# Performance work log

Hardware: AMD Instinct MI355X
Metric: run time of the kernel (lower is better)

## Reference

```python
import jax, jax.numpy as jnp
import numpy as np

B = 8          # graphs per batch
N_PER = 8192   # nodes per graph (equal-sized graphs -> static topk shapes)
N = B * N_PER  # 65536 total nodes
DEG = 16
E = DEG * N    # 1,048,576 edges
C = 64         # conv_width


def setup_inputs() -> dict:
    key = jax.random.key(0)
    ks = jax.random.split(key, 32)
    epg = E // B
    g = jnp.arange(E, dtype=jnp.int32) // epg            # graph id per edge
    src = jax.random.randint(ks[0], (E,), 0, N_PER, dtype=jnp.int32) + g * N_PER
    dst = jax.random.randint(ks[1], (E,), 0, N_PER, dtype=jnp.int32) + g * N_PER

    def w(k, shape, fan_in):
        return (jax.random.normal(k, shape) / np.sqrt(fan_in)).astype(jnp.float32)

    inp = {
        "x": jax.random.normal(ks[2], (N, 2), dtype=jnp.float32),
        "edge_index": jnp.stack([src, dst]),
        # SAGEConv i: out = mean_agg @ wl + x @ wr + b
        "w1l": w(ks[3], (2, C), 2),  "w1r": w(ks[4], (2, C), 2),  "b1": jnp.zeros((C,), jnp.float32),
        "w2l": w(ks[5], (C, C), C),  "w2r": w(ks[6], (C, C), C),  "b2": jnp.zeros((C,), jnp.float32),
        "w3l": w(ks[7], (C, C), C),  "w3r": w(ks[8], (C, C), C),  "b3": jnp.zeros((C,), jnp.float32),
        # GCNConv
        "w4": w(ks[9], (C, C), C),   "b4": jnp.zeros((C,), jnp.float32),
        # TopKPooling score vectors
        "p1": w(ks[10], (C,), C), "p2": w(ks[11], (C,), C),
        "p3": w(ks[12], (C,), C), "p4": w(ks[13], (C,), C),
        # MLP head
        "lw1": w(ks[14], (2 * C, 128), 2 * C), "lb1": jnp.zeros((128,), jnp.float32),
        "lw2": w(ks[15], (128, 64), 128),      "lb2": jnp.zeros((64,), jnp.float32),
        "lw3": w(ks[16], (64, 1), 64),         "lb3": jnp.zeros((1,), jnp.float32),
    }
    return inp


def _sage(x, src, dst, em, wl, wr, b):
    # PyG SAGEConv: lin_l(mean of in-neighbors) + lin_r(x); masked edges contribute 0
    n = x.shape[0]
    s = jax.ops.segment_sum(x[src] * em[:, None], dst, num_segments=n)
    cnt = jax.ops.segment_sum(em, dst, num_segments=n)
    mean = s / jnp.maximum(cnt, 1.0)[:, None]
    return mean @ wl + x @ wr + b


def _gcn(x, src, dst, em, w, b):
    # PyG GCNConv with added self-loops, symmetric normalization
    n = x.shape[0]
    xw = x @ w
    deg = jax.ops.segment_sum(em, dst, num_segments=n) + 1.0  # +1 self-loop
    dinv = jax.lax.rsqrt(deg)
    coef = (dinv[src] * dinv[dst] * em)[:, None]
    agg = jax.ops.segment_sum(xw[src] * coef, dst, num_segments=n)
    return agg + xw / deg[:, None] + b  # self-loop term: deg^-0.5 * deg^-0.5


def _pool(x, src, dst, em, p, nb):
    # TopKPooling(ratio=0.5): score = x.p/||p||, keep top half per graph, scale by tanh
    n = x.shape[0]
    npg = n // nb
    k = npg // 2
    score = x @ p / jnp.linalg.norm(p)
    _, idx = jax.lax.top_k(score.reshape(nb, npg), k)          # [nb, k] local idx
    perm = (idx + (jnp.arange(nb, dtype=idx.dtype) * npg)[:, None]).reshape(-1)
    xn = x[perm] * jnp.tanh(score[perm])[:, None]
    o2n = jnp.full((n,), -1, jnp.int32).at[perm].set(jnp.arange(nb * k, dtype=jnp.int32))
    ns, nd = o2n[src], o2n[dst]
    nm = em * ((ns >= 0) & (nd >= 0)).astype(em.dtype)         # filter_adj via mask
    return xn, jnp.maximum(ns, 0), jnp.maximum(nd, 0), nm


def _readout(x, nb):
    # cat([global_max_pool, global_mean_pool])
    npg = x.shape[0] // nb
    batch = jnp.repeat(jnp.arange(nb), npg)
    mx = jax.ops.segment_max(x, batch, num_segments=nb)
    mn = jax.ops.segment_sum(x, batch, num_segments=nb) / npg
    return jnp.concatenate([mx, mn], axis=1)


def reference(x, edge_index, w1l, w1r, b1, w2l, w2r, b2, w3l, w3r, b3, w4, b4,
              p1, p2, p3, p4, lw1, lb1, lw2, lb2, lw3, lb3):
    src, dst = edge_index[0], edge_index[1]
    em = jnp.ones((src.shape[0],), jnp.float32)

    h = jax.nn.relu(_sage(x, src, dst, em, w1l, w1r, b1))
    h, src, dst, em = _pool(h, src, dst, em, p1, B)
    x1 = _readout(h, B)

    h = jax.nn.relu(_sage(h, src, dst, em, w2l, w2r, b2))
    h, src, dst, em = _pool(h, src, dst, em, p2, B)
    x2 = _readout(h, B)

    h = jax.nn.relu(_sage(h, src, dst, em, w3l, w3r, b3))
    h, src, dst, em = _pool(h, src, dst, em, p3, B)
    x3 = _readout(h, B)  # computed but unused, matching original (x = x1 + x2)

    h = jax.nn.relu(_gcn(h, src, dst, em, w4, b4))
    h, src, dst, em = _pool(h, src, dst, em, p4, B)
    x4 = _readout(h, B)  # computed but unused, matching original

    z = x1 + x2
    z = jax.nn.relu(z @ lw1 + lb1)
    z = jax.nn.relu(z @ lw2 + lb2)
    return z @ lw3 + lb3  # [B, 1]
```

## Files before the change

### kernel.cpp

```cpp
#include <hip/hip_runtime.h>
#include <stdint.h>
#include <math.h>

#define NB 8
#define NPG0 8192
#define EPG 131072
#define P1 16
#define MAXDEG 64

__global__ __launch_bounds__(1024)
void k_aggp(const int* __restrict__ src, const int* __restrict__ dst,
            const float* __restrict__ x, float* __restrict__ partial)
{
    __shared__ float acc[3 * 2048];
    int b = blockIdx.x;
    int g = b >> 6, qq = (b >> 4) & 3, sl = b & 15;
    int tid = threadIdx.x;
    float4* acc4 = (float4*)acc;
    float4 z4 = make_float4(0.f, 0.f, 0.f, 0.f);
    acc4[tid] = z4;
    if (tid < 512) acc4[1024 + tid] = z4;
    __syncthreads();
    int e0 = g * EPG + sl * (EPG / P1);
    int nbase = g * NPG0 + qq * 2048;
    const float2* x2 = reinterpret_cast<const float2*>(x);
    #pragma unroll
    for (int k = 0; k < 2; ++k) {
        int e = e0 + (k * 1024 + tid) * 4;
        int4 d4 = *reinterpret_cast<const int4*>(dst + e);
        unsigned l0 = (unsigned)(d4.x - nbase), l1 = (unsigned)(d4.y - nbase);
        unsigned l2 = (unsigned)(d4.z - nbase), l3 = (unsigned)(d4.w - nbase);
        bool v0 = l0 < 2048u, v1 = l1 < 2048u, v2 = l2 < 2048u, v3 = l3 < 2048u;
        if (v0 | v1 | v2 | v3) {
            int4 s4 = *reinterpret_cast<const int4*>(src + e);
            if (v0) { float2 xv = x2[s4.x]; atomicAdd(&acc[l0], xv.x);
                      atomicAdd(&acc[2048 + l0], xv.y); atomicAdd(&acc[4096 + l0], 1.0f); }
            if (v1) { float2 xv = x2[s4.y]; atomicAdd(&acc[l1], xv.x);
                      atomicAdd(&acc[2048 + l1], xv.y); atomicAdd(&acc[4096 + l1], 1.0f); }
            if (v2) { float2 xv = x2[s4.z]; atomicAdd(&acc[l2], xv.x);
                      atomicAdd(&acc[2048 + l2], xv.y); atomicAdd(&acc[4096 + l2], 1.0f); }
            if (v3) { float2 xv = x2[s4.w]; atomicAdd(&acc[l3], xv.x);
                      atomicAdd(&acc[2048 + l3], xv.y); atomicAdd(&acc[4096 + l3], 1.0f); }
        }
    }
    __syncthreads();
    float4* o = (float4*)(partial + (size_t)b * 6144);
    o[tid] = acc4[tid];
    if (tid < 512) o[1024 + tid] = acc4[1024 + tid];
}

__global__ __launch_bounds__(256)
void k_sage1f(const float* __restrict__ partial, const float* __restrict__ x,
              const float* __restrict__ w1l, const float* __restrict__ w1r,
              const float* __restrict__ b1, const float* __restrict__ p1,
              float2* __restrict__ mv, float* __restrict__ s1)
{
    int tid = threadIdx.x;
    int node = blockIdx.x * 256 + tid;
    int g = node >> 13, local = node & (NPG0 - 1);
    int qq = local >> 11, ll = local & 2047;
    const float* p = partial + (size_t)(g * 64 + qq * 16) * 6144 + ll;
    float s0 = 0.f, s1v = 0.f, sc = 0.f;
    #pragma unroll
    for (int q = 0; q < 16; ++q) {
        const float* pq = p + (size_t)q * 6144;
        s0 += pq[0]; s1v += pq[2048]; sc += pq[4096];
    }
    float inv = 1.0f / fmaxf(sc, 1.0f);
    float m0 = s0 * inv, m1 = s1v * inv;
    float2 xv = reinterpret_cast<const float2*>(x)[node];
    mv[node] = make_float2(m0, m1);
    float num = 0.f, nrm = 0.f;
    #pragma unroll 8
    for (int c = 0; c < 64; ++c) {
        float h = fmaxf(m0 * w1l[c] + m1 * w1l[64 + c]
                      + xv.x * w1r[c] + xv.y * w1r[64 + c] + b1[c], 0.0f);
        float pv = p1[c];
        num += h * pv; nrm += pv * pv;
    }
    s1[node] = num / sqrtf(nrm);
}

__device__ __forceinline__ unsigned scan1024(unsigned val, volatile unsigned* ws)
{
    int tid = threadIdx.x, lane = tid & 63, wid = tid >> 6;
    unsigned sc = val;
    #pragma unroll
    for (int off = 1; off < 64; off <<= 1) {
        unsigned t = __shfl_up(sc, off);
        if (lane >= off) sc += t;
    }
    if (lane == 63) ws[wid] = sc;
    __syncthreads();
    if (tid < 16) {
        unsigned w = ws[tid];
        #pragma unroll
        for (int off = 1; off < 16; off <<= 1) {
            unsigned t = __shfl_up(w, off);
            if (tid >= off) w += t;
        }
        ws[tid] = w;
    }
    __syncthreads();
    return sc + (wid ? ws[wid - 1] : 0u);
}

template <int NPG>
__global__ __launch_bounds__(1024)
void k_pool_sel(const float* __restrict__ score, int* __restrict__ n2o,
                int* __restrict__ o2n, int K)
{
    __shared__ unsigned key[NPG];
    __shared__ unsigned hist[1024];
    __shared__ unsigned ws[16];
    __shared__ unsigned long long cand[1024];
    __shared__ int sT1, sR1, sT2, sR2, selCnt, c3;
    int g = blockIdx.x, tid = threadIdx.x;
    if (tid == 0) { selCnt = 0; c3 = 0; }
    hist[tid] = 0u;
    if (o2n) for (int i = tid; i < NPG; i += 1024) o2n[g * NPG + i] = -1;
    __syncthreads();
    for (int i = tid; i < NPG; i += 1024) {
        unsigned b = __float_as_uint(score[g * NPG + i]);
        unsigned u = (b & 0x80000000u) ? ~b : (b | 0x80000000u);
        key[i] = u;
        atomicAdd(&hist[u >> 22], 1u);
    }
    __syncthreads();
    {
        unsigned S = scan1024(hist[1023 - tid], ws);
        int b = 1023 - tid;
        unsigned h = hist[b];
        if (S >= (unsigned)K && S - h < (unsigned)K) { sT1 = b; sR1 = K - (int)(S - h); }
    }
    __syncthreads();
    int T1 = sT1, R1 = sR1;
    for (int i = tid; i < NPG; i += 1024) {
        if ((int)(key[i] >> 22) > T1) {
            int s = atomicAdd(&selCnt, 1);
            int oldid = g * NPG + i;
            n2o[g * K + s] = oldid;
            if (o2n) o2n[oldid] = g * K + s;
        }
    }
    __syncthreads();
    hist[tid] = 0u;
    __syncthreads();
    for (int i = tid; i < NPG; i += 1024)
        if ((int)(key[i] >> 22) == T1) atomicAdd(&hist[(key[i] >> 12) & 1023u], 1u);
    __syncthreads();
    {
        unsigned S = scan1024(hist[1023 - tid], ws);
        int b = 1023 - tid;
        unsigned h = hist[b];
        if (S >= (unsigned)R1 && S - h < (unsigned)R1) { sT2 = b; sR2 = R1 - (int)(S - h); }
    }
    __syncthreads();
    int T2 = sT2, R2 = sR2;
    for (int i = tid; i < NPG; i += 1024) {
        unsigned u = key[i];
        if ((int)(u >> 22) == T1) {
            int b2 = (int)((u >> 12) & 1023u);
            if (b2 > T2) {
                int s = atomicAdd(&selCnt, 1);
                int oldid = g * NPG + i;
                n2o[g * K + s] = oldid;
                if (o2n) o2n[oldid] = g * K + s;
            } else if (b2 == T2) {
                int c = atomicAdd(&c3, 1);
                if (c < 1024)
                    cand[c] = ((unsigned long long)u << 32) | (unsigned)(NPG - 1 - i);
            }
        }
    }
    __syncthreads();
    int M = min(c3, 1024);
    for (int t = tid; t < M; t += 1024) {
        unsigned long long k0 = cand[t];
        int rank = 0;
        for (int j = 0; j < M; ++j) rank += (cand[j] > k0);
        if (rank < R2) {
            int i = NPG - 1 - (int)(k0 & 0xFFFFFFFFu);
            int s = atomicAdd(&selCnt, 1);
            int oldid = g * NPG + i;
            n2o[g * K + s] = oldid;
            if (o2n) o2n[oldid] = g * K + s;
        }
    }
}

__global__ __launch_bounds__(1024)
void k_ro1(const float2* __restrict__ mv, const float* __restrict__ x,
           const float* __restrict__ s1, const int* __restrict__ n2o,
           const float* __restrict__ w1l, const float* __restrict__ w1r,
           const float* __restrict__ b1, int npg, float* __restrict__ hp,
           float* __restrict__ pmx, float* __restrict__ psm)
{
    int g = blockIdx.x >> 4, sl = blockIdx.x & 15;
    int tid = threadIdx.x;
    int cg = tid & 15, rsl = tid >> 4;
    int rpb = npg >> 4;
    int c0 = cg * 4;
    float4 wl0 = *reinterpret_cast<const float4*>(w1l + c0);
    float4 wl1 = *reinterpret_cast<const float4*>(w1l + 64 + c0);
    float4 wr0 = *reinterpret_cast<const float4*>(w1r + c0);
    float4 wr1 = *reinterpret_cast<const float4*>(w1r + 64 + c0);
    float4 bb  = *reinterpret_cast<const float4*>(b1 + c0);
    const float2* x2 = reinterpret_cast<const float2*>(x);
    float4 mx = make_float4(-INFINITY, -INFINITY, -INFINITY, -INFINITY);
    float4 sm = make_float4(0.f, 0.f, 0.f, 0.f);
    for (int r = rsl; r < rpb; r += 64) {
        int row = g * npg + sl * rpb + r;
        int old = n2o[row];
        float2 m = mv[old];
        float2 xv = x2[old];
        float t = tanhf(s1[old]);
        float4 v;
        v.x = fmaxf(m.x * wl0.x + m.y * wl1.x + xv.x * wr0.x + xv.y * wr1.x + bb.x, 0.f) * t;
        v.y = fmaxf(m.x * wl0.y + m.y * wl1.y + xv.x * wr0.y + xv.y * wr1.y + bb.y, 0.f) * t;
        v.z = fmaxf(m.x * wl0.z + m.y * wl1.z + xv.x * wr0.z + xv.y * wr1.z + bb.z, 0.f) * t;
        v.w = fmaxf(m.x * wl0.w + m.y * wl1.w + xv.x * wr0.w + xv.y * wr1.w + bb.w, 0.f) * t;
        reinterpret_cast<float4*>(hp)[row * 16 + cg] = v;
        mx.x = fmaxf(mx.x, v.x); mx.y = fmaxf(mx.y, v.y);
        mx.z = fmaxf(mx.z, v.z); mx.w = fmaxf(mx.w, v.w);
        sm.x += v.x; sm.y += v.y; sm.z += v.z; sm.w += v.w;
    }
    __shared__ float4 smx[1024], ssm[1024];
    smx[tid] = mx; ssm[tid] = sm;
    __syncthreads();
    for (int s = 32; s >= 1; s >>= 1) {
        if (rsl < s) {
            float4 a = smx[tid], b = smx[tid + s * 16];
            a.x = fmaxf(a.x, b.x); a.y = fmaxf(a.y, b.y);
            a.z = fmaxf(a.z, b.z); a.w = fmaxf(a.w, b.w);
            smx[tid] = a;
            float4 c = ssm[tid], d = ssm[tid + s * 16];
            c.x += d.x; c.y += d.y; c.z += d.z; c.w += d.w;
            ssm[tid] = c;
        }
        __syncthreads();
    }
    if (rsl == 0) {
        reinterpret_cast<float4*>(pmx)[(g * 16 + sl) * 16 + cg] = smx[tid];
        reinterpret_cast<float4*>(psm)[(g * 16 + sl) * 16 + cg] = ssm[tid];
    }
}

__global__ __launch_bounds__(1024)
void k_readout_p(const float* __restrict__ h, const int* __restrict__ n2o,
                 const float* __restrict__ sc, int npg,
                 float* __restrict__ pmx, float* __restrict__ psm)
{
    int g = blockIdx.x >> 4, sl = blockIdx.x & 15;
    int tid = threadIdx.x;
    int cg = tid & 15, rsl = tid >> 4;
    int rpb = npg >> 4;
    float4 mx = make_float4(-INFINITY, -INFINITY, -INFINITY, -INFINITY);
    float4 sm = make_float4(0.f, 0.f, 0.f, 0.f);
    for (int r = rsl; r < rpb; r += 64) {
        int row = g * npg + sl * rpb + r;
        int oldid = n2o ? n2o[row] : row;
        float4 v = reinterpret_cast<const float4*>(h)[oldid * 16 + cg];
        if (sc) {
            float t = tanhf(sc[oldid]);
            v.x *= t; v.y *= t; v.z *= t; v.w *= t;
        }
        mx.x = fmaxf(mx.x, v.x); mx.y = fmaxf(mx.y, v.y);
        mx.z = fmaxf(mx.z, v.z); mx.w = fmaxf(mx.w, v.w);
        sm.x += v.x; sm.y += v.y; sm.z += v.z; sm.w += v.w;
    }
    __shared__ float4 smx[1024], ssm[1024];
    smx[tid] = mx; ssm[tid] = sm;
    __syncthreads();
    for (int s = 32; s >= 1; s >>= 1) {
        if (rsl < s) {
            float4 a = smx[tid], b = smx[tid + s * 16];
            a.x = fmaxf(a.x, b.x); a.y = fmaxf(a.y, b.y);
            a.z = fmaxf(a.z, b.z); a.w = fmaxf(a.w, b.w);
            smx[tid] = a;
            float4 c = ssm[tid], d = ssm[tid + s * 16];
            c.x += d.x; c.y += d.y; c.z += d.z; c.w += d.w;
            ssm[tid] = c;
        }
        __syncthreads();
    }
    if (rsl == 0) {
        reinterpret_cast<float4*>(pmx)[(g * 16 + sl) * 16 + cg] = smx[tid];
        reinterpret_cast<float4*>(psm)[(g * 16 + sl) * 16 + cg] = ssm[tid];
    }
}

__global__ void k_build(const int* __restrict__ src, const int* __restrict__ dst,
                        const int* __restrict__ o2n, int* __restrict__ cnt,
                        int* __restrict__ slots, int E)
{
    int e = (blockIdx.x * 256 + threadIdx.x) * 4;
    if (e >= E) return;
    int4 s4 = *reinterpret_cast<const int4*>(src + e);
    int4 d4 = *reinterpret_cast<const int4*>(dst + e);
    #pragma unroll
    for (int i = 0; i < 4; ++i) {
        int sv = (i == 0) ? s4.x : (i == 1) ? s4.y : (i == 2) ? s4.z : s4.w;
        int dv = (i == 0) ? d4.x : (i == 1) ? d4.y : (i == 2) ? d4.z : d4.w;
        int ns = o2n[sv], nd = o2n[dv];
        if (ns >= 0 && nd >= 0) {
            int pos = atomicAdd(&cnt[nd], 1);
            if (pos < MAXDEG) slots[nd * MAXDEG + pos] = ns;
        }
    }
}

__global__ __launch_bounds__(256)
void k_sage2(const float* __restrict__ hp, const int* __restrict__ cnt,
             const int* __restrict__ slots,
             const float* __restrict__ w2l, const float* __restrict__ w2r,
             const float* __restrict__ b2, const float* __restrict__ p2,
             float* __restrict__ h2, float* __restrict__ s2)
{
    __shared__ float Xs[64 * 128];
    __shared__ float Wt[64 * 128];
    int tid = threadIdx.x, blk = blockIdx.x;

    #pragma unroll
    for (int i = 0; i < 32; ++i) {
        int idx = i * 256 + tid;
        int k = idx >> 6, c = idx & 63;
        float w = (k < 64) ? w2l[k * 64 + c] : w2r[(k - 64) * 64 + c];
        int slot = (k >> 2) ^ ((c >> 2) & 7);
        Wt[c * 128 + slot * 4 + (k & 3)] = w;
    }

    {
        int n = tid >> 2, p = tid & 3;
        int j = blk * 64 + n;
        int dg = cnt[j];
        int lim = min(dg, MAXDEG);
        const int* sl = slots + j * MAXDEG;
        const float4* hp4 = reinterpret_cast<const float4*>(hp);
        float4 a[4];
        #pragma unroll
        for (int u = 0; u < 4; ++u) a[u] = make_float4(0.f, 0.f, 0.f, 0.f);
        int e = 0;
        for (; e + 1 < lim; e += 2) {
            int r0 = sl[e] * 16 + p * 4;
            int r1 = sl[e + 1] * 16 + p * 4;
            float4 v[4], u4[4];
            #pragma unroll
            for (int u = 0; u < 4; ++u) v[u] = hp4[r0 + u];
            #pragma unroll
            for (int u = 0; u < 4; ++u) u4[u] = hp4[r1 + u];
            #pragma unroll
            for (int u = 0; u < 4; ++u) {
                a[u].x += v[u].x + u4[u].x; a[u].y += v[u].y + u4[u].y;
                a[u].z += v[u].z + u4[u].z; a[u].w += v[u].w + u4[u].w;
            }
        }
        if (e < lim) {
            int r0 = sl[e] * 16 + p * 4;
            #pragma unroll
            for (int u = 0; u < 4; ++u) {
                float4 v = hp4[r0 + u];
                a[u].x += v.x; a[u].y += v.y; a[u].z += v.z; a[u].w += v.w;
            }
        }
        float inv = 1.0f / fmaxf((float)dg, 1.0f);
        int swz = (n >> 2) & 7;
        float4* X4 = reinterpret_cast<float4*>(Xs);
        #pragma unroll
        for (int u = 0; u < 4; ++u) {
            float4 m = a[u];
            m.x *= inv; m.y *= inv; m.z *= inv; m.w *= inv;
            X4[n * 32 + ((p * 4 + u) ^ swz)] = m;
        }
        #pragma unroll
        for (int u = 0; u < 4; ++u)
            X4[n * 32 + ((16 + p * 4 + u) ^ swz)] = hp4[j * 16 + p * 4 + u];
    }
    __syncthreads();

    int rt = tid >> 4, ct = tid & 15;
    int r0 = rt * 4, c0 = ct * 4;
    int swa = rt & 7, swb = ct & 7;
    const float4* Xf = reinterpret_cast<const float4*>(Xs);
    const float4* Wf = reinterpret_cast<const float4*>(Wt);
    float acc[4][4];
    #pragma unroll
    for (int i = 0; i < 4; ++i)
        #pragma unroll
        for (int jq = 0; jq < 4; ++jq) acc[i][jq] = 0.f;
    #pragma unroll 8
    for (int ks = 0; ks < 32; ++ks) {
        float4 aa[4], bb[4];
        #pragma unroll
        for (int i = 0; i < 4; ++i) aa[i] = Xf[(r0 + i) * 32 + (ks ^ swa)];
        #pragma unroll
        for (int jq = 0; jq < 4; ++jq) bb[jq] = Wf[(c0 + jq) * 32 + (ks ^ swb)];
        #pragma unroll
        for (int i = 0; i < 4; ++i)
            #pragma unroll
            for (int jq = 0; jq < 4; ++jq)
                acc[i][jq] += aa[i].x * bb[jq].x + aa[i].y * bb[jq].y
                            + aa[i].z * bb[jq].z + aa[i].w * bb[jq].w;
    }

    float4 b2v = reinterpret_cast<const float4*>(b2)[ct];
    float4 p2v = reinterpret_cast<const float4*>(p2)[ct];
    float nrm = p2v.x * p2v.x + p2v.y * p2v.y + p2v.z * p2v.z + p2v.w * p2v.w;
    float sp[4];
    float4* h2f = reinterpret_cast<float4*>(h2);
    #pragma unroll
    for (int i = 0; i < 4; ++i) {
        float4 o;
        o.x = fmaxf(acc[i][0] + b2v.x, 0.f);
        o.y = fmaxf(acc[i][1] + b2v.y, 0.f);
        o.z = fmaxf(acc[i][2] + b2v.z, 0.f);
        o.w = fmaxf(acc[i][3] + b2v.w, 0.f);
        h2f[(blk * 64 + r0 + i) * 16 + ct] = o;
        sp[i] = o.x * p2v.x + o.y * p2v.y + o.z * p2v.z + o.w * p2v.w;
    }
    #pragma unroll
    for (int o = 1; o < 16; o <<= 1) {
        #pragma unroll
        for (int i = 0; i < 4; ++i) sp[i] += __shfl_xor(sp[i], o);
        nrm += __shfl_xor(nrm, o);
    }
    if (ct == 0) {
        float r = rsqrtf(nrm);
        #pragma unroll
        for (int i = 0; i < 4; ++i) s2[blk * 64 + r0 + i] = sp[i] * r;
    }
}

__global__ __launch_bounds__(128)
void k_mlp(const float* __restrict__ pmx1, const float* __restrict__ psm1,
           const float* __restrict__ pmx2, const float* __restrict__ psm2,
           int npg1, int npg2,
           const float* __restrict__ lw1, const float* __restrict__ lb1,
           const float* __restrict__ lw2, const float* __restrict__ lb2,
           const float* __restrict__ lw3, const float* __restrict__ lb3,
           float* __restrict__ out)
{
    __shared__ float z[NB][128], o1[NB][128], o2[NB][64];
    int tid = threadIdx.x;
    for (int g = 0; g < NB; ++g) {
        float v;
        if (tid < 64) {
            float m1 = -INFINITY, m2 = -INFINITY;
            #pragma unroll
            for (int sl = 0; sl < 16; ++sl) {
                m1 = fmaxf(m1, pmx1[(g * 16 + sl) * 64 + tid]);
                m2 = fmaxf(m2, pmx2[(g * 16 + sl) * 64 + tid]);
            }
            v = m1 + m2;
        } else {
            int ch = tid - 64;
            float s1 = 0.f, s2 = 0.f;
            #pragma unroll
            for (int sl = 0; sl < 16; ++sl) {
                s1 += psm1[(g * 16 + sl) * 64 + ch];
                s2 += psm2[(g * 16 + sl) * 64 + ch];
            }
            v = s1 / (float)npg1 + s2 / (float)npg2;
        }
        z[g][tid] = v;
    }
    __syncthreads();
    for (int g = 0; g < NB; ++g) {
        float a = lb1[tid];
        for (int i = 0; i < 128; ++i) a += z[g][i] * lw1[i * 128 + tid];
        o1[g][tid] = fmaxf(a, 0.0f);
    }
    __syncthreads();
    if (tid < 64) {
        for (int g = 0; g < NB; ++g) {
            float a = lb2[tid];
            for (int i = 0; i < 128; ++i) a += o1[g][i] * lw2[i * 64 + tid];
            o2[g][tid] = fmaxf(a, 0.0f);
        }
    }
    __syncthreads();
    if (tid < NB) {
        int g = tid;
        float a = lb3[0];
        for (int i = 0; i < 64; ++i) a += o2[g][i] * lw3[i];
        out[g] = a;
    }
}

extern "C" void kernel_launch(void* const* d_in, const int* in_sizes, int n_in,
                              void* d_out, int out_size, void* d_ws, size_t ws_size,
                              hipStream_t stream)
{
    (void)n_in; (void)out_size; (void)ws_size;
    const float* x   = (const float*)d_in[0];
    const int*   ei  = (const int*)d_in[1];
    const float* w1l = (const float*)d_in[2];
    const float* w1r = (const float*)d_in[3];
    const float* b1  = (const float*)d_in[4];
    const float* w2l = (const float*)d_in[5];
    const float* w2r = (const float*)d_in[6];
    const float* b2  = (const float*)d_in[7];
    const float* p1  = (const float*)d_in[13];
    const float* p2  = (const float*)d_in[14];
    const float* lw1 = (const float*)d_in[17];
    const float* lb1 = (const float*)d_in[18];
    const float* lw2 = (const float*)d_in[19];
    const float* lb2 = (const float*)d_in[20];
    const float* lw3 = (const float*)d_in[21];
    const float* lb3 = (const float*)d_in[22];

    const int N0   = in_sizes[0] / 2;
    const int E    = in_sizes[1] / 2;
    const int K1   = NPG0 / 2;
    const int N1   = NB * K1;
    const int K2   = K1 / 2;

    const int* src = ei;
    const int* dst = ei + E;

    char* w = (char*)d_ws;
    auto alloc = [&](size_t bytes) -> char* {
        char* p = w;
        w += (bytes + 255) & ~(size_t)255;
        return p;
    };
    float*  partial = (float*)alloc((size_t)NB * 4 * P1 * 6144 * 4);
    float2* mv    = (float2*)alloc((size_t)N0 * 8);
    int*    cnt2  = (int*)alloc((size_t)N1 * 4);
    int*    slots = (int*)alloc((size_t)N1 * MAXDEG * 4);
    float*  s1    = (float*)alloc((size_t)N0 * 4);
    int*    o2n1  = (int*)alloc((size_t)N0 * 4);
    int*    n2o1  = (int*)alloc((size_t)N1 * 4);
    float*  h1p   = (float*)alloc((size_t)N1 * 64 * 4);
    float*  h2    = (float*)alloc((size_t)N1 * 64 * 4);
    float*  s2    = (float*)alloc((size_t)N1 * 4);
    int*    n2o2  = (int*)alloc((size_t)(NB * K2) * 4);
    float*  pmx1  = (float*)alloc((size_t)NB * 16 * 64 * 4);
    float*  psm1  = (float*)alloc((size_t)NB * 16 * 64 * 4);
    float*  pmx2  = (float*)alloc((size_t)NB * 16 * 64 * 4);
    float*  psm2  = (float*)alloc((size_t)NB * 16 * 64 * 4);

    hipMemsetAsync(cnt2, 0, (size_t)N1 * 4, stream);

    k_aggp<<<NB * 4 * P1, 1024, 0, stream>>>(src, dst, x, partial);
    k_sage1f<<<N0 / 256, 256, 0, stream>>>(partial, x, w1l, w1r, b1, p1, mv, s1);
    k_pool_sel<8192><<<NB, 1024, 0, stream>>>(s1, n2o1, o2n1, K1);
    k_ro1<<<NB * 16, 1024, 0, stream>>>(mv, x, s1, n2o1, w1l, w1r, b1, K1,
                                        h1p, pmx1, psm1);
    k_build<<<E / 1024, 256, 0, stream>>>(src, dst, o2n1, cnt2, slots, E);
    k_sage2<<<N1 / 64, 256, 0, stream>>>(h1p, cnt2, slots, w2l, w2r, b2, p2, h2, s2);
    k_pool_sel<4096><<<NB, 1024, 0, stream>>>(s2, n2o2, nullptr, K2);
    k_readout_p<<<NB * 16, 1024, 0, stream>>>(h2, n2o2, s2, K2, pmx2, psm2);
    k_mlp<<<1, 128, 0, stream>>>(pmx1, psm1, pmx2, psm2, K1, K2,
                                 lw1, lb1, lw2, lb2, lw3, lb3, (float*)d_out);
}
```

Measured before the change: 135.0 us.

## Fuse pooling, readout and edge-build kernels and drop the memset launch

Merges the edge-list rebuild into the layer-1 readout kernel as extra blocks, and folds the cnt2 zeroing into the first pool kernel in place of a separate memset. The second pooling now does its selection and readout in one kernel with a shared-memory index list, emitting final per-graph features directly. Stage 1 aggregation now covers 4096-node halves with larger shared accumulators, so there are fewer partial blocks per graph. The aim is to cut launch count and intermediate traffic, at the cost of more shared memory per block and only 8 blocks in the fused pool/readout kernel.

```diff
diff --git a/kernel.cpp b/kernel.cpp
--- a/kernel.cpp
+++ b/kernel.cpp
@@ -5,24 +5,23 @@
 #define NB 8
 #define NPG0 8192
 #define EPG 131072
-#define P1 16
 #define MAXDEG 64
 
 __global__ __launch_bounds__(1024)
 void k_aggp(const int* __restrict__ src, const int* __restrict__ dst,
             const float* __restrict__ x, float* __restrict__ partial)
 {
-    __shared__ float acc[3 * 2048];
+    __shared__ float acc[3 * 4096];
     int b = blockIdx.x;
-    int g = b >> 6, qq = (b >> 4) & 3, sl = b & 15;
+    int g = b >> 5, hh = (b >> 4) & 1, sl = b & 15;
     int tid = threadIdx.x;
     float4* acc4 = (float4*)acc;
     float4 z4 = make_float4(0.f, 0.f, 0.f, 0.f);
-    acc4[tid] = z4;
-    if (tid < 512) acc4[1024 + tid] = z4;
-    __syncthreads();
-    int e0 = g * EPG + sl * (EPG / P1);
-    int nbase = g * NPG0 + qq * 2048;
+    #pragma unroll
+    for (int i = 0; i < 3; ++i) acc4[i * 1024 + tid] = z4;
+    __syncthreads();
+    int e0 = g * EPG + sl * (EPG / 16);
+    int nbase = g * NPG0 + hh * 4096;
     const float2* x2 = reinterpret_cast<const float2*>(x);
     #pragma unroll
     for (int k = 0; k < 2; ++k) {
@@ -30,23 +29,23 @@
         int4 d4 = *reinterpret_cast<const int4*>(dst + e);
         unsigned l0 = (unsigned)(d4.x - nbase), l1 = (unsigned)(d4.y - nbase);
         unsigned l2 = (unsigned)(d4.z - nbase), l3 = (unsigned)(d4.w - nbase);
-        bool v0 = l0 < 2048u, v1 = l1 < 2048u, v2 = l2 < 2048u, v3 = l3 < 2048u;
+        bool v0 = l0 < 4096u, v1 = l1 < 4096u, v2 = l2 < 4096u, v3 = l3 < 4096u;
         if (v0 | v1 | v2 | v3) {
             int4 s4 = *reinterpret_cast<const int4*>(src + e);
             if (v0) { float2 xv = x2[s4.x]; atomicAdd(&acc[l0], xv.x);
-                      atomicAdd(&acc[2048 + l0], xv.y); atomicAdd(&acc[4096 + l0], 1.0f); }
+                      atomicAdd(&acc[4096 + l0], xv.y); atomicAdd(&acc[8192 + l0], 1.0f); }
             if (v1) { float2 xv = x2[s4.y]; atomicAdd(&acc[l1], xv.x);
-                      atomicAdd(&acc[2048 + l1], xv.y); atomicAdd(&acc[4096 + l1], 1.0f); }
+                      atomicAdd(&acc[4096 + l1], xv.y); atomicAdd(&acc[8192 + l1], 1.0f); }
             if (v2) { float2 xv = x2[s4.z]; atomicAdd(&acc[l2], xv.x);
-                      atomicAdd(&acc[2048 + l2], xv.y); atomicAdd(&acc[4096 + l2], 1.0f); }
+                      atomicAdd(&acc[4096 + l2], xv.y); atomicAdd(&acc[8192 + l2], 1.0f); }
             if (v3) { float2 xv = x2[s4.w]; atomicAdd(&acc[l3], xv.x);
-                      atomicAdd(&acc[2048 + l3], xv.y); atomicAdd(&acc[4096 + l3], 1.0f); }
-        }
-    }
-    __syncthreads();
-    float4* o = (float4*)(partial + (size_t)b * 6144);
-    o[tid] = acc4[tid];
-    if (tid < 512) o[1024 + tid] = acc4[1024 + tid];
+                      atomicAdd(&acc[4096 + l3], xv.y); atomicAdd(&acc[8192 + l3], 1.0f); }
+        }
+    }
+    __syncthreads();
+    float4* o = (float4*)(partial + (size_t)b * 12288);
+    #pragma unroll
+    for (int i = 0; i < 3; ++i) o[i * 1024 + tid] = acc4[i * 1024 + tid];
 }
 
 __global__ __launch_bounds__(256)
@@ -58,13 +57,13 @@
     int tid = threadIdx.x;
     int node = blockIdx.x * 256 + tid;
     int g = node >> 13, local = node & (NPG0 - 1);
-    int qq = local >> 11, ll = local & 2047;
-    const float* p = partial + (size_t)(g * 64 + qq * 16) * 6144 + ll;
+    int hh = local >> 12, ll = local & 4095;
+    const float* p = partial + (size_t)(g * 32 + hh * 16) * 12288 + ll;
     float s0 = 0.f, s1v = 0.f, sc = 0.f;
     #pragma unroll
     for (int q = 0; q < 16; ++q) {
-        const float* pq = p + (size_t)q * 6144;
-        s0 += pq[0]; s1v += pq[2048]; sc += pq[4096];
+        const float* pq = p + (size_t)q * 12288;
+        s0 += pq[0]; s1v += pq[4096]; sc += pq[8192];
     }
     float inv = 1.0f / fmaxf(sc, 1.0f);
     float m0 = s0 * inv, m1 = s1v * inv;
@@ -105,20 +104,21 @@
     return sc + (wid ? ws[wid - 1] : 0u);
 }
 
-template <int NPG>
 __global__ __launch_bounds__(1024)
-void k_pool_sel(const float* __restrict__ score, int* __restrict__ n2o,
-                int* __restrict__ o2n, int K)
-{
+void k_pool1(const float* __restrict__ score, int* __restrict__ n2o,
+             int* __restrict__ o2n, int K, int* __restrict__ zbuf)
+{
+    const int NPG = 8192;
     __shared__ unsigned key[NPG];
     __shared__ unsigned hist[1024];
     __shared__ unsigned ws[16];
     __shared__ unsigned long long cand[1024];
     __shared__ int sT1, sR1, sT2, sR2, selCnt, c3;
     int g = blockIdx.x, tid = threadIdx.x;
+    for (int i = tid; i < 4096; i += 1024) zbuf[g * 4096 + i] = 0;
     if (tid == 0) { selCnt = 0; c3 = 0; }
     hist[tid] = 0u;
-    if (o2n) for (int i = tid; i < NPG; i += 1024) o2n[g * NPG + i] = -1;
+    for (int i = tid; i < NPG; i += 1024) o2n[g * NPG + i] = -1;
     __syncthreads();
     for (int i = tid; i < NPG; i += 1024) {
         unsigned b = __float_as_uint(score[g * NPG + i]);
@@ -140,7 +140,7 @@
             int s = atomicAdd(&selCnt, 1);
             int oldid = g * NPG + i;
             n2o[g * K + s] = oldid;
-            if (o2n) o2n[oldid] = g * K + s;
+            o2n[oldid] = g * K + s;
         }
     }
     __syncthreads();
@@ -165,7 +165,7 @@
                 int s = atomicAdd(&selCnt, 1);
                 int oldid = g * NPG + i;
                 n2o[g * K + s] = oldid;
-                if (o2n) o2n[oldid] = g * K + s;
+                o2n[oldid] = g * K + s;
             } else if (b2 == T2) {
                 int c = atomicAdd(&c3, 1);
                 if (c < 1024)
@@ -184,20 +184,41 @@
             int s = atomicAdd(&selCnt, 1);
             int oldid = g * NPG + i;
             n2o[g * K + s] = oldid;
-            if (o2n) o2n[oldid] = g * K + s;
+            o2n[oldid] = g * K + s;
         }
     }
 }
 
 __global__ __launch_bounds__(1024)
-void k_ro1(const float2* __restrict__ mv, const float* __restrict__ x,
+void k_mid(const float2* __restrict__ mv, const float* __restrict__ x,
            const float* __restrict__ s1, const int* __restrict__ n2o,
            const float* __restrict__ w1l, const float* __restrict__ w1r,
            const float* __restrict__ b1, int npg, float* __restrict__ hp,
-           float* __restrict__ pmx, float* __restrict__ psm)
-{
-    int g = blockIdx.x >> 4, sl = blockIdx.x & 15;
+           float* __restrict__ pmx, float* __restrict__ psm,
+           const int* __restrict__ src, const int* __restrict__ dst,
+           const int* __restrict__ o2n, int* __restrict__ cnt,
+           int* __restrict__ slots)
+{
+    __shared__ float4 smx[1024], ssm[1024];
+    int b = blockIdx.x;
     int tid = threadIdx.x;
+    if (b >= 128) {
+        int e = ((b - 128) * 1024 + tid) * 4;
+        int4 s4 = *reinterpret_cast<const int4*>(src + e);
+        int4 d4 = *reinterpret_cast<const int4*>(dst + e);
+        #pragma unroll
+        for (int i = 0; i < 4; ++i) {
+            int sv = (i == 0) ? s4.x : (i == 1) ? s4.y : (i == 2) ? s4.z : s4.w;
+            int dv = (i == 0) ? d4.x : (i == 1) ? d4.y : (i == 2) ? d4.z : d4.w;
+            int ns = o2n[sv], nd = o2n[dv];
+            if (ns >= 0 && nd >= 0) {
+                int pos = atomicAdd(&cnt[nd], 1);
+                if (pos < MAXDEG) slots[nd * MAXDEG + pos] = ns;
+            }
+        }
+        return;
+    }
+    int g = b >> 4, sl = b & 15;
     int cg = tid & 15, rsl = tid >> 4;
     int rpb = npg >> 4;
     int c0 = cg * 4;
@@ -225,14 +246,13 @@
         mx.z = fmaxf(mx.z, v.z); mx.w = fmaxf(mx.w, v.w);
         sm.x += v.x; sm.y += v.y; sm.z += v.z; sm.w += v.w;
     }
-    __shared__ float4 smx[1024], ssm[1024];
     smx[tid] = mx; ssm[tid] = sm;
     __syncthreads();
     for (int s = 32; s >= 1; s >>= 1) {
         if (rsl < s) {
-            float4 a = smx[tid], b = smx[tid + s * 16];
-            a.x = fmaxf(a.x, b.x); a.y = fmaxf(a.y, b.y);
-            a.z = fmaxf(a.z, b.z); a.w = fmaxf(a.w, b.w);
+            float4 a = smx[tid], bq = smx[tid + s * 16];
+            a.x = fmaxf(a.x, bq.x); a.y = fmaxf(a.y, bq.y);
+            a.z = fmaxf(a.z, bq.z); a.w = fmaxf(a.w, bq.w);
             smx[tid] = a;
             float4 c = ssm[tid], d = ssm[tid + s * 16];
             c.x += d.x; c.y += d.y; c.z += d.z; c.w += d.w;
@@ -243,70 +263,6 @@
     if (rsl == 0) {
         reinterpret_cast<float4*>(pmx)[(g * 16 + sl) * 16 + cg] = smx[tid];
         reinterpret_cast<float4*>(psm)[(g * 16 + sl) * 16 + cg] = ssm[tid];
-    }
-}
-
-__global__ __launch_bounds__(1024)
-void k_readout_p(const float* __restrict__ h, const int* __restrict__ n2o,
-                 const float* __restrict__ sc, int npg,
-                 float* __restrict__ pmx, float* __restrict__ psm)
-{
-    int g = blockIdx.x >> 4, sl = blockIdx.x & 15;
-    int tid = threadIdx.x;
-    int cg = tid & 15, rsl = tid >> 4;
-    int rpb = npg >> 4;
-    float4 mx = make_float4(-INFINITY, -INFINITY, -INFINITY, -INFINITY);
-    float4 sm = make_float4(0.f, 0.f, 0.f, 0.f);
-    for (int r = rsl; r < rpb; r += 64) {
-        int row = g * npg + sl * rpb + r;
-        int oldid = n2o ? n2o[row] : row;
-        float4 v = reinterpret_cast<const float4*>(h)[oldid * 16 + cg];
-        if (sc) {
-            float t = tanhf(sc[oldid]);
-            v.x *= t; v.y *= t; v.z *= t; v.w *= t;
-        }
-        mx.x = fmaxf(mx.x, v.x); mx.y = fmaxf(mx.y, v.y);
-        mx.z = fmaxf(mx.z, v.z); mx.w = fmaxf(mx.w, v.w);
-        sm.x += v.x; sm.y += v.y; sm.z += v.z; sm.w += v.w;
-    }
-    __shared__ float4 smx[1024], ssm[1024];
-    smx[tid] = mx; ssm[tid] = sm;
-    __syncthreads();
-    for (int s = 32; s >= 1; s >>= 1) {
-        if (rsl < s) {
-            float4 a = smx[tid], b = smx[tid + s * 16];
-            a.x = fmaxf(a.x, b.x); a.y = fmaxf(a.y, b.y);
-            a.z = fmaxf(a.z, b.z); a.w = fmaxf(a.w, b.w);
-            smx[tid] = a;
-            float4 c = ssm[tid], d = ssm[tid + s * 16];
-            c.x += d.x; c.y += d.y; c.z += d.z; c.w += d.w;
-            ssm[tid] = c;
-        }
-        __syncthreads();
-    }
-    if (rsl == 0) {
-        reinterpret_cast<float4*>(pmx)[(g * 16 + sl) * 16 + cg] = smx[tid];
-        reinterpret_cast<float4*>(psm)[(g * 16 + sl) * 16 + cg] = ssm[tid];
-    }
-}
-
-__global__ void k_build(const int* __restrict__ src, const int* __restrict__ dst,
-                        const int* __restrict__ o2n, int* __restrict__ cnt,
-                        int* __restrict__ slots, int E)
-{
-    int e = (blockIdx.x * 256 + threadIdx.x) * 4;
-    if (e >= E) return;
-    int4 s4 = *reinterpret_cast<const int4*>(src + e);
-    int4 d4 = *reinterpret_cast<const int4*>(dst + e);
-    #pragma unroll
-    for (int i = 0; i < 4; ++i) {
-        int sv = (i == 0) ? s4.x : (i == 1) ? s4.y : (i == 2) ? s4.z : s4.w;
-        int dv = (i == 0) ? d4.x : (i == 1) ? d4.y : (i == 2) ? d4.z : d4.w;
-        int ns = o2n[sv], nd = o2n[dv];
-        if (ns >= 0 && nd >= 0) {
-            int pos = atomicAdd(&cnt[nd], 1);
-            if (pos < MAXDEG) slots[nd * MAXDEG + pos] = ns;
-        }
     }
 }
 
@@ -431,10 +387,114 @@
     }
 }
 
+__global__ __launch_bounds__(1024)
+void k_pool_ro2(const float* __restrict__ score, const float* __restrict__ h2,
+                float* __restrict__ x2v)
+{
+    const int NPG = 4096, K = 2048;
+    __shared__ unsigned key[NPG];
+    __shared__ unsigned hist[1024];
+    __shared__ unsigned ws[16];
+    __shared__ unsigned long long cand[1024];
+    __shared__ int n2oL[K];
+    __shared__ int sT1, sR1, sT2, sR2, selCnt, c3;
+    __shared__ float4 smx[1024], ssm[1024];
+    int g = blockIdx.x, tid = threadIdx.x;
+    if (tid == 0) { selCnt = 0; c3 = 0; }
+    hist[tid] = 0u;
+    __syncthreads();
+    for (int i = tid; i < NPG; i += 1024) {
+        unsigned b = __float_as_uint(score[g * NPG + i]);
+        unsigned u = (b & 0x80000000u) ? ~b : (b | 0x80000000u);
+        key[i] = u;
+        atomicAdd(&hist[u >> 22], 1u);
+    }
+    __syncthreads();
+    {
+        unsigned S = scan1024(hist[1023 - tid], ws);
+        int b = 1023 - tid;
+        unsigned h = hist[b];
+        if (S >= (unsigned)K && S - h < (unsigned)K) { sT1 = b; sR1 = K - (int)(S - h); }
+    }
+    __syncthreads();
+    int T1 = sT1, R1 = sR1;
+    for (int i = tid; i < NPG; i += 1024) {
+        if ((int)(key[i] >> 22) > T1) n2oL[atomicAdd(&selCnt, 1)] = i;
+    }
+    __syncthreads();
+    hist[tid] = 0u;
+    __syncthreads();
+    for (int i = tid; i < NPG; i += 1024)
+        if ((int)(key[i] >> 22) == T1) atomicAdd(&hist[(key[i] >> 12) & 1023u], 1u);
+    __syncthreads();
+    {
+        unsigned S = scan1024(hist[1023 - tid], ws);
+        int b = 1023 - tid;
+        unsigned h = hist[b];
+        if (S >= (unsigned)R1 && S - h < (unsigned)R1) { sT2 = b; sR2 = R1 - (int)(S - h); }
+    }
+    __syncthreads();
+    int T2 = sT2, R2 = sR2;
+    for (int i = tid; i < NPG; i += 1024) {
+        unsigned u = key[i];
+        if ((int)(u >> 22) == T1) {
+            int b2 = (int)((u >> 12) & 1023u);
+            if (b2 > T2) {
+                n2oL[atomicAdd(&selCnt, 1)] = i;
+            } else if (b2 == T2) {
+                int c = atomicAdd(&c3, 1);
+                if (c < 1024)
+                    cand[c] = ((unsigned long long)u << 32) | (unsigned)(NPG - 1 - i);
+            }
+        }
+    }
+    __syncthreads();
+    int M = min(c3, 1024);
+    for (int t = tid; t < M; t += 1024) {
+        unsigned long long k0 = cand[t];
+        int rank = 0;
+        for (int j = 0; j < M; ++j) rank += (cand[j] > k0);
+        if (rank < R2) n2oL[atomicAdd(&selCnt, 1)] = NPG - 1 - (int)(k0 & 0xFFFFFFFFu);
+    }
+    __syncthreads();
+    int cg = tid & 15, rsl = tid >> 4;
+    float4 mx = make_float4(-INFINITY, -INFINITY, -INFINITY, -INFINITY);
+    float4 sm = make_float4(0.f, 0.f, 0.f, 0.f);
+    for (int r = rsl; r < K; r += 64) {
+        int old = g * NPG + n2oL[r];
+        float t = tanhf(score[old]);
+        float4 v = reinterpret_cast<const float4*>(h2)[old * 16 + cg];
+        v.x *= t; v.y *= t; v.z *= t; v.w *= t;
+        mx.x = fmaxf(mx.x, v.x); mx.y = fmaxf(mx.y, v.y);
+        mx.z = fmaxf(mx.z, v.z); mx.w = fmaxf(mx.w, v.w);
+        sm.x += v.x; sm.y += v.y; sm.z += v.z; sm.w += v.w;
+    }
+    smx[tid] = mx; ssm[tid] = sm;
+    __syncthreads();
+    for (int s = 32; s >= 1; s >>= 1) {
+        if (rsl < s) {
+            float4 a = smx[tid], bq = smx[tid + s * 16];
+            a.x = fmaxf(a.x, bq.x); a.y = fmaxf(a.y, bq.y);
+            a.z = fmaxf(a.z, bq.z); a.w = fmaxf(a.w, bq.w);
+            smx[tid] = a;
+            float4 c = ssm[tid], d = ssm[tid + s * 16];
+            c.x += d.x; c.y += d.y; c.z += d.z; c.w += d.w;
+            ssm[tid] = c;
+        }
+        __syncthreads();
+    }
+    if (rsl == 0) {
+        float4 m = smx[tid], s = ssm[tid];
+        float* o = x2v + g * 128 + cg * 4;
+        o[0] = m.x; o[1] = m.y; o[2] = m.z; o[3] = m.w;
+        float invK = 1.0f / (float)K;
+        o[64] = s.x * invK; o[65] = s.y * invK; o[66] = s.z * invK; o[67] = s.w * invK;
+    }
+}
+
 __global__ __launch_bounds__(128)
 void k_mlp(const float* __restrict__ pmx1, const float* __restrict__ psm1,
-           const float* __restrict__ pmx2, const float* __restrict__ psm2,
-           int npg1, int npg2,
+           const float* __restrict__ x2v, int npg1,
            const float* __restrict__ lw1, const float* __restrict__ lb1,
            const float* __restrict__ lw2, const float* __restrict__ lb2,
            const float* __restrict__ lw3, const float* __restrict__ lb3,
@@ -445,24 +505,20 @@
     for (int g = 0; g < NB; ++g) {
         float v;
         if (tid < 64) {
-            float m1 = -INFINITY, m2 = -INFINITY;
+            float m1 = -INFINITY;
             #pragma unroll
-            for (int sl = 0; sl < 16; ++sl) {
+            for (int sl = 0; sl < 16; ++sl)
                 m1 = fmaxf(m1, pmx1[(g * 16 + sl) * 64 + tid]);
-                m2 = fmaxf(m2, pmx2[(g * 16 + sl) * 64 + tid]);
-            }
-            v = m1 + m2;
+            v = m1;
         } else {
             int ch = tid - 64;
-            float s1 = 0.f, s2 = 0.f;
+            float s1 = 0.f;
             #pragma unroll
-            for (int sl = 0; sl < 16; ++sl) {
+            for (int sl = 0; sl < 16; ++sl)
                 s1 += psm1[(g * 16 + sl) * 64 + ch];
-                s2 += psm2[(g * 16 + sl) * 64 + ch];
-            }
-            v = s1 / (float)npg1 + s2 / (float)npg2;
-        }
-        z[g][tid] = v;
+            v = s1 / (float)npg1;
+        }
+        z[g][tid] = v + x2v[g * 128 + tid];
     }
     __syncthreads();
     for (int g = 0; g < NB; ++g) {
@@ -513,7 +569,6 @@
     const int E    = in_sizes[1] / 2;
     const int K1   = NPG0 / 2;
     const int N1   = NB * K1;
-    const int K2   = K1 / 2;
 
     const int* src = ei;
     const int* dst = ei + E;
@@ -524,7 +579,7 @@
         w += (bytes + 255) & ~(size_t)255;
         return p;
     };
-    float*  partial = (float*)alloc((size_t)NB * 4 * P1 * 6144 * 4);
+    float*  partial = (float*)alloc((size_t)NB * 2 * 16 * 12288 * 4);
     float2* mv    = (float2*)alloc((size_t)N0 * 8);
     int*    cnt2  = (int*)alloc((size_t)N1 * 4);
     int*    slots = (int*)alloc((size_t)N1 * MAXDEG * 4);
@@ -534,23 +589,18 @@
     float*  h1p   = (float*)alloc((size_t)N1 * 64 * 4);
     float*  h2    = (float*)alloc((size_t)N1 * 64 * 4);
     float*  s2    = (float*)alloc((size_t)N1 * 4);
-    int*    n2o2  = (int*)alloc((size_t)(NB * K2) * 4);
     float*  pmx1  = (float*)alloc((size_t)NB * 16 * 64 * 4);
     float*  psm1  = (float*)alloc((size_t)NB * 16 * 64 * 4);
-    float*  pmx2  = (float*)alloc((size_t)NB * 16 * 64 * 4);
-    float*  psm2  = (float*)alloc((size_t)NB * 16 * 64 * 4);
-
-    hipMemsetAsync(cnt2, 0, (size_t)N1 * 4, stream);
-
-    k_aggp<<<NB * 4 * P1, 1024, 0, stream>>>(src, dst, x, partial);
+    float*  x2v   = (float*)alloc((size_t)NB * 128 * 4);
+
+    k_aggp<<<NB * 2 * 16, 1024, 0, stream>>>(src, dst, x, partial);
     k_sage1f<<<N0 / 256, 256, 0, stream>>>(partial, x, w1l, w1r, b1, p1, mv, s1);
-    k_pool_sel<8192><<<NB, 1024, 0, stream>>>(s1, n2o1, o2n1, K1);
-    k_ro1<<<NB * 16, 1024, 0, stream>>>(mv, x, s1, n2o1, w1l, w1r, b1, K1,
-                                        h1p, pmx1, psm1);
-    k_build<<<E / 1024, 256, 0, stream>>>(src, dst, o2n1, cnt2, slots, E);
+    k_pool1<<<NB, 1024, 0, stream>>>(s1, n2o1, o2n1, K1, cnt2);
+    k_mid<<<128 + 256, 1024, 0, stream>>>(mv, x, s1, n2o1, w1l, w1r, b1, K1,
+                                          h1p, pmx1, psm1,
+                                          src, dst, o2n1, cnt2, slots);
     k_sage2<<<N1 / 64, 256, 0, stream>>>(h1p, cnt2, slots, w2l, w2r, b2, p2, h2, s2);
-    k_pool_sel<4096><<<NB, 1024, 0, stream>>>(s2, n2o2, nullptr, K2);
-    k_readout_p<<<NB * 16, 1024, 0, stream>>>(h2, n2o2, s2, K2, pmx2, psm2);
-    k_mlp<<<1, 128, 0, stream>>>(pmx1, psm1, pmx2, psm2, K1, K2,
+    k_pool_ro2<<<NB, 1024, 0, stream>>>(s2, h2, x2v);
+    k_mlp<<<1, 128, 0, stream>>>(pmx1, psm1, x2v, K1,
                                  lw1, lb1, lw2, lb2, lw3, lb3, (float*)d_out);
 }
```

New measurement: 141.5 us. 4.8% more time.
